# Performance work log

Measured on AMD Instinct MI355X. Metric: run time of the kernel, lower is better.

## Reference

```python
import jax, jax.numpy as jnp
import numpy as np

B, N, E, H = 8, 10000, 320000, 128


def setup_inputs() -> dict:
    key = jax.random.key(0)
    ks = jax.random.split(key, 8)
    x = jax.random.normal(ks[0], (B, N, H), dtype=jnp.float32)
    adj_val = jnp.ones((B, E), dtype=jnp.float32)
    src = jax.random.randint(ks[1], (B, E), 0, N, dtype=jnp.int32)
    dst = jax.random.randint(ks[2], (B, E), 0, N, dtype=jnp.int32)
    scale = 0.05  # 'random_normal' keras initializer default stddev
    W_t = scale * jax.random.normal(ks[3], (H, H), dtype=jnp.float32)
    b_t = jnp.zeros((H,), dtype=jnp.float32)
    W_h = scale * jax.random.normal(ks[4], (H, H), dtype=jnp.float32)
    theta = scale * jax.random.normal(ks[5], (H, H), dtype=jnp.float32)
    return {"x": x, "adj_val": adj_val, "src": src, "dst": dst,
            "W_t": W_t, "b_t": b_t, "W_h": W_h, "theta": theta}


def reference(x, adj_val, src, dst, W_t, b_t, W_h, theta):
    # adj is sparse [B, N, N]: adj[b, src[b,e], dst[b,e]] = adj_val[b,e]
    n = x.shape[1]
    # in_degrees = row-sums of adj
    deg = jax.vmap(lambda v, s: jax.ops.segment_sum(v, s, num_segments=n))(adj_val, src)
    norm = jnp.power(deg + 1e-6, -0.5)[..., None]            # [B, N, 1]
    f_hom = jnp.einsum('bnh,hk->bnk', x, theta) * norm       # [B, N, H]
    # batched SpMM: out[b,i] = sum_e adj_val[b,e] * y[b, dst[b,e]] into row src[b,e]
    def spmm(v, s, d, y):
        return jax.ops.segment_sum(v[:, None] * y[d], s, num_segments=n)
    f_hom = jax.vmap(spmm)(adj_val, src, dst, f_hom) * norm  # [B, N, H]
    f_het = jnp.einsum('bnh,hk->bnk', x, W_h)
    gate = jax.nn.sigmoid(jnp.einsum('bnh,hk->bnk', x, W_t) + b_t)
    return gate * f_hom + (1.0 - gate) * f_het
```

## Files before the change

### kernel.cpp

```cpp
#include <hip/hip_runtime.h>

#define BATCH 8
#define NNODE 10000
#define NEDGE 320000
#define HD    128
#define NROW  (BATCH * NNODE)
#define NEDG_TOT (BATCH * NEDGE)
#define LDW 136
#define KB  32
#define CEB (NEDGE / KB)
#define G   64
#define NBUCK 157
#define NBP 160
#define NBT (BATCH * NBP)
#define WCVT_B 192

typedef __attribute__((ext_vector_type(8))) short short8;
typedef __attribute__((ext_vector_type(4))) float f32x4;

__device__ __forceinline__ short f2bf(float f) {
    unsigned u = __float_as_uint(f);
    unsigned r = u + 0x7FFFu + ((u >> 16) & 1u);
    return (short)(r >> 16);
}
__device__ __forceinline__ float bflo(unsigned y) { return __uint_as_float(y << 16); }
__device__ __forceinline__ float bfhi(unsigned y) { return __uint_as_float(y & 0xffff0000u); }

__global__ __launch_bounds__(512) void k_hist(const int* __restrict__ src,
                                              int* __restrict__ cc) {
    __shared__ int scc[NBP];
    int t = threadIdx.x, blk = blockIdx.x;
    if (t < NBP) scc[t] = 0;
    __syncthreads();
    int b = blk >> 5, kb = blk & (KB - 1);
    long e0 = (long)b * NEDGE + (long)kb * CEB;
    for (int i0 = t; i0 < CEB; i0 += 2048) {
        int i1 = i0 + 512, i2 = i0 + 1024, i3 = i0 + 1536;
        int s0 = src[e0 + i0];
        int s1 = (i1 < CEB) ? src[e0 + i1] : -1;
        int s2 = (i2 < CEB) ? src[e0 + i2] : -1;
        int s3 = (i3 < CEB) ? src[e0 + i3] : -1;
        atomicAdd(&scc[s0 >> 6], 1);
        if (s1 >= 0) atomicAdd(&scc[s1 >> 6], 1);
        if (s2 >= 0) atomicAdd(&scc[s2 >> 6], 1);
        if (s3 >= 0) atomicAdd(&scc[s3 >> 6], 1);
    }
    __syncthreads();
    if (t < NBP) cc[blk * NBP + t] = scc[t];
}

__global__ __launch_bounds__(256) void k_misc(const float* __restrict__ th,
                                              const float* __restrict__ Wt,
                                              const float* __restrict__ Wh,
                                              short* __restrict__ wbf,
                                              int* __restrict__ cc,
                                              int* __restrict__ tot_c,
                                              int* __restrict__ cbaseA,
                                              int* __restrict__ cbaseB) {
    __shared__ int partA[256], partB[256];
    int t = threadIdx.x, blk = blockIdx.x;
    if (blk < WCVT_B) {
        int i = blk * 256 + t;
        int w = i >> 14, idx = i & 16383;
        int n = idx >> 7, k = idx & 127;
        const float* W = (w == 0) ? th : ((w == 1) ? Wt : Wh);
        wbf[i] = f2bf(W[k * HD + n]);
    } else {
        int tot[5], locA[5], locB[5]; int runA = 0, runB = 0;
        #pragma unroll
        for (int j = 0; j < 5; ++j) {
            int gi = t * 5 + j, b = gi / NBP, bk = gi % NBP;
            int s = 0;
            for (int k = 0; k < KB; ++k) s += cc[(b * KB + k) * NBP + bk];
            tot[j] = s;
            locA[j] = runA; runA += s;
            locB[j] = runB; runB += (s + 3 * G + 3) & ~3;
        }
        partA[t] = runA; partB[t] = runB; __syncthreads();
        for (int off = 1; off < 256; off <<= 1) {
            int a = partA[t], bb = partB[t];
            int aa = (t >= off) ? partA[t - off] : 0;
            int ab = (t >= off) ? partB[t - off] : 0;
            __syncthreads();
            partA[t] = a + aa; partB[t] = bb + ab;
            __syncthreads();
        }
        int exA = (t == 0) ? 0 : partA[t - 1];
        int exB = (t == 0) ? 0 : partB[t - 1];
        #pragma unroll
        for (int j = 0; j < 5; ++j) {
            int gi = t * 5 + j, b = gi / NBP, bk = gi % NBP;
            tot_c[gi]  = tot[j];
            cbaseA[gi] = exA + locA[j];
            cbaseB[gi] = exB + locB[j];
            int run2 = exA + locA[j];
            for (int k = 0; k < KB; ++k) {
                int idx = (b * KB + k) * NBP + bk;
                int c = cc[idx];
                cc[idx] = run2;
                run2 += c;
            }
        }
    }
}

__global__ __launch_bounds__(512) void k_scatA(const float* __restrict__ adj,
                                               const int* __restrict__ src,
                                               const int* __restrict__ dst,
                                               const int* __restrict__ cbases,
                                               int2* __restrict__ epairA) {
    __shared__ int cur[NBP];
    int t = threadIdx.x, blk = blockIdx.x;
    if (t < NBP) cur[t] = cbases[blk * NBP + t];
    __syncthreads();
    int b = blk >> 5, kb = blk & (KB - 1);
    long e0 = (long)b * NEDGE + (long)kb * CEB;
    for (int i0 = t; i0 < CEB; i0 += 2048) {
        int i1 = i0 + 512, i2 = i0 + 1024, i3 = i0 + 1536;
        int s0 = src[e0 + i0], d0 = dst[e0 + i0];
        float a0 = adj[e0 + i0];
        int s1 = -1, d1 = 0; float a1 = 0.f;
        int s2 = -1, d2 = 0; float a2 = 0.f;
        int s3 = -1, d3 = 0; float a3 = 0.f;
        if (i1 < CEB) { s1 = src[e0 + i1]; d1 = dst[e0 + i1]; a1 = adj[e0 + i1]; }
        if (i2 < CEB) { s2 = src[e0 + i2]; d2 = dst[e0 + i2]; a2 = adj[e0 + i2]; }
        if (i3 < CEB) { s3 = src[e0 + i3]; d3 = dst[e0 + i3]; a3 = adj[e0 + i3]; }
        int p0 = atomicAdd(&cur[s0 >> 6], 1);
        epairA[p0] = make_int2((s0 << 16) | d0, __float_as_int(a0));
        if (s1 >= 0) {
            int p1 = atomicAdd(&cur[s1 >> 6], 1);
            epairA[p1] = make_int2((s1 << 16) | d1, __float_as_int(a1));
        }
        if (s2 >= 0) {
            int p2 = atomicAdd(&cur[s2 >> 6], 1);
            epairA[p2] = make_int2((s2 << 16) | d2, __float_as_int(a2));
        }
        if (s3 >= 0) {
            int p3 = atomicAdd(&cur[s3 >> 6], 1);
            epairA[p3] = make_int2((s3 << 16) | d3, __float_as_int(a3));
        }
    }
}

__global__ __launch_bounds__(256) void k_refine(const int* __restrict__ cbaseA,
                                                const int* __restrict__ cbaseB,
                                                const int* __restrict__ tot_c,
                                                const int2* __restrict__ epairA,
                                                int* __restrict__ rowptr,
                                                int* __restrict__ total,
                                                float* __restrict__ norm,
                                                int* __restrict__ epakB) {
    __shared__ int   rcnt[G];
    __shared__ float sdeg[G];
    __shared__ int   rcur[G];
    int t = threadIdx.x;
    int batch = blockIdx.x & 7, bk = blockIdx.x >> 3;
    if (t < G) { rcnt[t] = 0; sdeg[t] = 0.f; }
    __syncthreads();
    int gi = batch * NBP + bk;
    int p0 = cbaseA[gi], n = tot_c[gi], pB = cbaseB[gi];
    for (int i = t; i < n; i += 256) {
        int2 e = epairA[p0 + i];
        int rl = (e.x >> 16) & (G - 1);
        atomicAdd(&rcnt[rl], 1);
        atomicAdd(&sdeg[rl], __int_as_float(e.y));
    }
    __syncthreads();
    if (t < G) {
        int v = rcnt[t];
        int pv = (v + 3) & ~3;
        int inc = pv;
        #pragma unroll
        for (int off = 1; off < G; off <<= 1) {
            int u = __shfl_up(inc, off, G);
            if (t >= off) inc += u;
        }
        int start = pB + inc - pv;
        rcur[t] = start;
        int node = bk * G + t;
        if (node < NNODE) {
            long r = (long)batch * NNODE + node;
            rowptr[r] = start;
            total[r] = v;
            norm[r] = rsqrtf(sdeg[t] + 1e-6f);
        }
    }
    __syncthreads();
    for (int i = t; i < n; i += 256) {
        int2 e = epairA[p0 + i];
        int rl = (e.x >> 16) & (G - 1);
        int p = atomicAdd(&rcur[rl], 1);
        unsigned vbf = (unsigned short)f2bf(__int_as_float(e.y));
        epakB[p] = (e.x & 0xffff) | (vbf << 16);
    }
}

__global__ __launch_bounds__(256) void k_gemm3(const float* __restrict__ x,
                                               const short* __restrict__ wbf,
                                               const float* __restrict__ norm,
                                               const float* __restrict__ bt,
                                               short* __restrict__ Y,
                                               unsigned* __restrict__ outgh) {
    __shared__ short lb[2 * HD * LDW];
    int tx = threadIdx.x;
    for (int i = tx; i < HD * 16; i += 256) {
        int n = i >> 4, kc = (i & 15) << 3;
        *(float4*)(&lb[n * LDW + kc])            = *(const float4*)(&wbf[n * HD + kc]);
        *(float4*)(&lb[HD * LDW + n * LDW + kc]) = *(const float4*)(&wbf[16384 + n * HD + kc]);
    }
    __syncthreads();

    int wv = tx >> 6, l = tx & 63;
    long row0 = (long)blockIdx.x * 64 + wv * 16;
    int mrow = l & 15, kg = l >> 4;
    const float* xp = x + (row0 + mrow) * HD + kg * 8;

    f32x4 ac0[8], ac1[8];
    #pragma unroll
    for (int f = 0; f < 8; ++f) { ac0[f] = (f32x4){0.f,0.f,0.f,0.f}; ac1[f] = (f32x4){0.f,0.f,0.f,0.f}; }

    #pragma unroll
    for (int c = 0; c < 4; ++c) {
        float4 a0 = *(const float4*)(xp + c * 32);
        float4 a1 = *(const float4*)(xp + c * 32 + 4);
        short8 a;
        a[0]=f2bf(a0.x); a[1]=f2bf(a0.y); a[2]=f2bf(a0.z); a[3]=f2bf(a0.w);
        a[4]=f2bf(a1.x); a[5]=f2bf(a1.y); a[6]=f2bf(a1.z); a[7]=f2bf(a1.w);
        #pragma unroll
        for (int f = 0; f < 8; ++f) {
            short8 b0 = *(short8*)(&lb[(16 * f + mrow) * LDW + c * 32 + kg * 8]);
            short8 b1 = *(short8*)(&lb[HD * LDW + (16 * f + mrow) * LDW + c * 32 + kg * 8]);
            ac0[f] = __builtin_amdgcn_mfma_f32_16x16x32_bf16(a, b0, ac0[f], 0, 0, 0);
            ac1[f] = __builtin_amdgcn_mfma_f32_16x16x32_bf16(a, b1, ac1[f], 0, 0, 0);
        }
    }
    float nr[4];
    #pragma unroll
    for (int r = 0; r < 4; ++r) nr[r] = norm[row0 + kg * 4 + r];
    #pragma unroll
    for (int f = 0; f < 8; ++f)
        #pragma unroll
        for (int r = 0; r < 4; ++r)
            Y[(row0 + kg * 4 + r) * HD + 16 * f + mrow] = f2bf(ac0[f][r] * nr[r]);

    __syncthreads();
    for (int i = tx; i < HD * 16; i += 256) {
        int n = i >> 4, kc = (i & 15) << 3;
        *(float4*)(&lb[n * LDW + kc]) = *(const float4*)(&wbf[2 * 16384 + n * HD + kc]);
    }
    __syncthreads();

    f32x4 ac2[8];
    #pragma unroll
    for (int f = 0; f < 8; ++f) ac2[f] = (f32x4){0.f,0.f,0.f,0.f};
    #pragma unroll
    for (int c = 0; c < 4; ++c) {
        float4 a0 = *(const float4*)(xp + c * 32);
        float4 a1 = *(const float4*)(xp + c * 32 + 4);
        short8 a;
        a[0]=f2bf(a0.x); a[1]=f2bf(a0.y); a[2]=f2bf(a0.z); a[3]=f2bf(a0.w);
        a[4]=f2bf(a1.x); a[5]=f2bf(a1.y); a[6]=f2bf(a1.z); a[7]=f2bf(a1.w);
        #pragma unroll
        for (int f = 0; f < 8; ++f) {
            short8 b = *(short8*)(&lb[(16 * f + mrow) * LDW + c * 32 + kg * 8]);
            ac2[f] = __builtin_amdgcn_mfma_f32_16x16x32_bf16(a, b, ac2[f], 0, 0, 0);
        }
    }
    #pragma unroll
    for (int f = 0; f < 8; ++f) {
        float bb = bt[16 * f + mrow];
        #pragma unroll
        for (int r = 0; r < 4; ++r) {
            long idx = (row0 + kg * 4 + r) * HD + 16 * f + mrow;
            float g = 1.f / (1.f + __expf(-(ac1[f][r] + bb)));
            unsigned glo = (unsigned short)f2bf(g);
            unsigned hhi = (unsigned short)f2bf(ac2[f][r]);
            outgh[idx] = glo | (hhi << 16);
        }
    }
}

__global__ __launch_bounds__(256) void k_gather(const int* __restrict__ rowptr,
                                                const int* __restrict__ total,
                                                const int* __restrict__ epak,
                                                const short* __restrict__ Y,
                                                const float* __restrict__ norm,
                                                float* __restrict__ out) {
    int batch = blockIdx.x & 7;
    int ib    = blockIdx.x >> 3;
    int wave = threadIdx.x >> 6, lane = threadIdx.x & 63;
    long r = (long)batch * NNODE + ib * 4 + wave;
    const short* Yb = Y + (long)batch * NNODE * HD + 2 * lane;
    int p0 = __builtin_amdgcn_readfirstlane(rowptr[r]);
    int n  = __builtin_amdgcn_readfirstlane(total[r]);
    const int* ep = epak + p0;
    float ax = 0.f, ay = 0.f;
    int i = 0;
    for (; i + 16 <= n; i += 16) {
        int4 mA = *(const int4*)(ep + i);
        int4 mB = *(const int4*)(ep + i + 4);
        int4 mC = *(const int4*)(ep + i + 8);
        int4 mD = *(const int4*)(ep + i + 12);
        unsigned y0 = *(const unsigned*)(Yb + (long)(mA.x & 0xffff) * HD);
        unsigned y1 = *(const unsigned*)(Yb + (long)(mA.y & 0xffff) * HD);
        unsigned y2 = *(const unsigned*)(Yb + (long)(mA.z & 0xffff) * HD);
        unsigned y3 = *(const unsigned*)(Yb + (long)(mA.w & 0xffff) * HD);
        unsigned y4 = *(const unsigned*)(Yb + (long)(mB.x & 0xffff) * HD);
        unsigned y5 = *(const unsigned*)(Yb + (long)(mB.y & 0xffff) * HD);
        unsigned y6 = *(const unsigned*)(Yb + (long)(mB.z & 0xffff) * HD);
        unsigned y7 = *(const unsigned*)(Yb + (long)(mB.w & 0xffff) * HD);
        unsigned y8 = *(const unsigned*)(Yb + (long)(mC.x & 0xffff) * HD);
        unsigned y9 = *(const unsigned*)(Yb + (long)(mC.y & 0xffff) * HD);
        unsigned yA = *(const unsigned*)(Yb + (long)(mC.z & 0xffff) * HD);
        unsigned yB = *(const unsigned*)(Yb + (long)(mC.w & 0xffff) * HD);
        unsigned yC = *(const unsigned*)(Yb + (long)(mD.x & 0xffff) * HD);
        unsigned yD = *(const unsigned*)(Yb + (long)(mD.y & 0xffff) * HD);
        unsigned yE = *(const unsigned*)(Yb + (long)(mD.z & 0xffff) * HD);
        unsigned yF = *(const unsigned*)(Yb + (long)(mD.w & 0xffff) * HD);
        float v0 = bfhi((unsigned)mA.x), v1 = bfhi((unsigned)mA.y);
        float v2 = bfhi((unsigned)mA.z), v3 = bfhi((unsigned)mA.w);
        float v4 = bfhi((unsigned)mB.x), v5 = bfhi((unsigned)mB.y);
        float v6 = bfhi((unsigned)mB.z), v7 = bfhi((unsigned)mB.w);
        float v8 = bfhi((unsigned)mC.x), v9 = bfhi((unsigned)mC.y);
        float vA = bfhi((unsigned)mC.z), vB = bfhi((unsigned)mC.w);
        float vC = bfhi((unsigned)mD.x), vD = bfhi((unsigned)mD.y);
        float vE = bfhi((unsigned)mD.z), vF = bfhi((unsigned)mD.w);
        ax += v0 * bflo(y0); ay += v0 * bfhi(y0);
        ax += v1 * bflo(y1); ay += v1 * bfhi(y1);
        ax += v2 * bflo(y2); ay += v2 * bfhi(y2);
        ax += v3 * bflo(y3); ay += v3 * bfhi(y3);
        ax += v4 * bflo(y4); ay += v4 * bfhi(y4);
        ax += v5 * bflo(y5); ay += v5 * bfhi(y5);
        ax += v6 * bflo(y6); ay += v6 * bfhi(y6);
        ax += v7 * bflo(y7); ay += v7 * bfhi(y7);
        ax += v8 * bflo(y8); ay += v8 * bfhi(y8);
        ax += v9 * bflo(y9); ay += v9 * bfhi(y9);
        ax += vA * bflo(yA); ay += vA * bfhi(yA);
        ax += vB * bflo(yB); ay += vB * bfhi(yB);
        ax += vC * bflo(yC); ay += vC * bfhi(yC);
        ax += vD * bflo(yD); ay += vD * bfhi(yD);
        ax += vE * bflo(yE); ay += vE * bfhi(yE);
        ax += vF * bflo(yF); ay += vF * bfhi(yF);
    }
    for (; i + 4 <= n; i += 4) {
        int4 mA = *(const int4*)(ep + i);
        unsigned y0 = *(const unsigned*)(Yb + (long)(mA.x & 0xffff) * HD);
        unsigned y1 = *(const unsigned*)(Yb + (long)(mA.y & 0xffff) * HD);
        unsigned y2 = *(const unsigned*)(Yb + (long)(mA.z & 0xffff) * HD);
        unsigned y3 = *(const unsigned*)(Yb + (long)(mA.w & 0xffff) * HD);
        float v0 = bfhi((unsigned)mA.x), v1 = bfhi((unsigned)mA.y);
        float v2 = bfhi((unsigned)mA.z), v3 = bfhi((unsigned)mA.w);
        ax += v0 * bflo(y0); ay += v0 * bfhi(y0);
        ax += v1 * bflo(y1); ay += v1 * bfhi(y1);
        ax += v2 * bflo(y2); ay += v2 * bfhi(y2);
        ax += v3 * bflo(y3); ay += v3 * bfhi(y3);
    }
    for (; i < n; ++i) {
        unsigned e = (unsigned)ep[i];
        unsigned y = *(const unsigned*)(Yb + (long)(e & 0xffff) * HD);
        float v = bfhi(e);
        ax += v * bflo(y); ay += v * bfhi(y);
    }
    float nrm = norm[r];
    uint2 gh = ((const uint2*)(out + r * HD))[lane];
    float g0 = bflo(gh.x), h0 = bfhi(gh.x);
    float g1 = bflo(gh.y), h1 = bfhi(gh.y);
    float z0 = ax * nrm, z1 = ay * nrm;
    ((float2*)(out + r * HD))[lane] =
        make_float2(g0 * z0 + (1.f - g0) * h0, g1 * z1 + (1.f - g1) * h1);
}

extern "C" void kernel_launch(void* const* d_in, const int* in_sizes, int n_in,
                              void* d_out, int out_size, void* d_ws, size_t ws_size,
                              hipStream_t stream) {
    const float* x     = (const float*)d_in[0];
    const float* adj   = (const float*)d_in[1];
    const int*   src   = (const int*)d_in[2];
    const int*   dst   = (const int*)d_in[3];
    const float* Wt    = (const float*)d_in[4];
    const float* bt    = (const float*)d_in[5];
    const float* Wh    = (const float*)d_in[6];
    const float* theta = (const float*)d_in[7];
    float* out = (float*)d_out;

    char* p = (char*)d_ws;
    float* norm   = (float*)p;  p += (size_t)NROW * 4;
    int*   total  = (int*)p;    p += (size_t)NROW * 4;
    int*   rowptr = (int*)p;    p += (size_t)NROW * 4;
    int*   tot_c  = (int*)p;    p += (size_t)NBT * 4;
    int*   cbaseA = (int*)p;    p += (size_t)NBT * 4;
    int*   cbaseB = (int*)p;    p += (size_t)NBT * 4;
    int*   cc     = (int*)p;    p += (size_t)BATCH * KB * NBP * 4;
    short* wbf    = (short*)p;  p += 3 * 16384 * 2;
    int2*  epairA = (int2*)p;
    short* Y      = (short*)p;  p += (size_t)NROW * HD * 2;
    int*   epakB  = (int*)p;    p += (size_t)(NEDG_TOT + NBT * 256) * 4;

    k_hist  <<<BATCH * KB, 512, 0, stream>>>(src, cc);
    k_misc  <<<WCVT_B + 1, 256, 0, stream>>>(theta, Wt, Wh, wbf, cc, tot_c, cbaseA, cbaseB);
    k_scatA <<<BATCH * KB, 512, 0, stream>>>(adj, src, dst, cc, epairA);
    k_refine<<<BATCH * NBUCK, 256, 0, stream>>>(cbaseA, cbaseB, tot_c, epairA,
                                                rowptr, total, norm, epakB);
    k_gemm3 <<<NROW / 64, 256, 0, stream>>>(x, wbf, norm, bt, Y, (unsigned*)out);
    k_gather<<<NROW / 4, 256, 0, stream>>>(rowptr, total, epakB, Y, norm, out);
}
```

Baseline: 152.7 us.

## Run GEMM phases sequentially with one LDS weight buffer and cached bf16 A fragments

The fused three-weight GEMM kernel now loads one 128x128 bf16 weight matrix into LDS at a time, halving shared memory, and runs the theta, W_t and W_h products one after another with a single accumulator set. The x rows are converted to bf16 once and held in registers instead of being reloaded and reconverted for the last GEMM, and gate values are packed into 16 registers between phases. This lowers LDS and accumulator register use to allow more resident blocks, at the cost of extra barriers and serialized weight loads.

```diff
diff --git a/kernel.cpp b/kernel.cpp
--- a/kernel.cpp
+++ b/kernel.cpp
@@ -201,24 +201,14 @@
                                                const float* __restrict__ bt,
                                                short* __restrict__ Y,
                                                unsigned* __restrict__ outgh) {
-    __shared__ short lb[2 * HD * LDW];
+    __shared__ short lb[HD * LDW];
     int tx = threadIdx.x;
-    for (int i = tx; i < HD * 16; i += 256) {
-        int n = i >> 4, kc = (i & 15) << 3;
-        *(float4*)(&lb[n * LDW + kc])            = *(const float4*)(&wbf[n * HD + kc]);
-        *(float4*)(&lb[HD * LDW + n * LDW + kc]) = *(const float4*)(&wbf[16384 + n * HD + kc]);
-    }
-    __syncthreads();
-
     int wv = tx >> 6, l = tx & 63;
     long row0 = (long)blockIdx.x * 64 + wv * 16;
     int mrow = l & 15, kg = l >> 4;
     const float* xp = x + (row0 + mrow) * HD + kg * 8;
 
-    f32x4 ac0[8], ac1[8];
-    #pragma unroll
-    for (int f = 0; f < 8; ++f) { ac0[f] = (f32x4){0.f,0.f,0.f,0.f}; ac1[f] = (f32x4){0.f,0.f,0.f,0.f}; }
-
+    short8 af[4];
     #pragma unroll
     for (int c = 0; c < 4; ++c) {
         float4 a0 = *(const float4*)(xp + c * 32);
@@ -226,14 +216,24 @@
         short8 a;
         a[0]=f2bf(a0.x); a[1]=f2bf(a0.y); a[2]=f2bf(a0.z); a[3]=f2bf(a0.w);
         a[4]=f2bf(a1.x); a[5]=f2bf(a1.y); a[6]=f2bf(a1.z); a[7]=f2bf(a1.w);
+        af[c] = a;
+    }
+
+    for (int i = tx; i < HD * 16; i += 256) {
+        int n = i >> 4, kc = (i & 15) << 3;
+        *(float4*)(&lb[n * LDW + kc]) = *(const float4*)(&wbf[n * HD + kc]);
+    }
+    __syncthreads();
+    f32x4 ac[8];
+    #pragma unroll
+    for (int f = 0; f < 8; ++f) ac[f] = (f32x4){0.f,0.f,0.f,0.f};
+    #pragma unroll
+    for (int c = 0; c < 4; ++c)
         #pragma unroll
         for (int f = 0; f < 8; ++f) {
-            short8 b0 = *(short8*)(&lb[(16 * f + mrow) * LDW + c * 32 + kg * 8]);
-            short8 b1 = *(short8*)(&lb[HD * LDW + (16 * f + mrow) * LDW + c * 32 + kg * 8]);
-            ac0[f] = __builtin_amdgcn_mfma_f32_16x16x32_bf16(a, b0, ac0[f], 0, 0, 0);
-            ac1[f] = __builtin_amdgcn_mfma_f32_16x16x32_bf16(a, b1, ac1[f], 0, 0, 0);
-        }
-    }
+            short8 b = *(short8*)(&lb[(16 * f + mrow) * LDW + c * 32 + kg * 8]);
+            ac[f] = __builtin_amdgcn_mfma_f32_16x16x32_bf16(af[c], b, ac[f], 0, 0, 0);
+        }
     float nr[4];
     #pragma unroll
     for (int r = 0; r < 4; ++r) nr[r] = norm[row0 + kg * 4 + r];
@@ -241,7 +241,36 @@
     for (int f = 0; f < 8; ++f)
         #pragma unroll
         for (int r = 0; r < 4; ++r)
-            Y[(row0 + kg * 4 + r) * HD + 16 * f + mrow] = f2bf(ac0[f][r] * nr[r]);
+            Y[(row0 + kg * 4 + r) * HD + 16 * f + mrow] = f2bf(ac[f][r] * nr[r]);
+
+    __syncthreads();
+    for (int i = tx; i < HD * 16; i += 256) {
+        int n = i >> 4, kc = (i & 15) << 3;
+        *(float4*)(&lb[n * LDW + kc]) = *(const float4*)(&wbf[16384 + n * HD + kc]);
+    }
+    __syncthreads();
+    #pragma unroll
+    for (int f = 0; f < 8; ++f) ac[f] = (f32x4){0.f,0.f,0.f,0.f};
+    #pragma unroll
+    for (int c = 0; c < 4; ++c)
+        #pragma unroll
+        for (int f = 0; f < 8; ++f) {
+            short8 b = *(short8*)(&lb[(16 * f + mrow) * LDW + c * 32 + kg * 8]);
+            ac[f] = __builtin_amdgcn_mfma_f32_16x16x32_bf16(af[c], b, ac[f], 0, 0, 0);
+        }
+    unsigned g16[16];
+    #pragma unroll
+    for (int f = 0; f < 8; ++f) {
+        float bb = bt[16 * f + mrow];
+        #pragma unroll
+        for (int r = 0; r < 4; ++r) {
+            int q = f * 4 + r;
+            float g = 1.f / (1.f + __expf(-(ac[f][r] + bb)));
+            unsigned gb = (unsigned short)f2bf(g);
+            if (q & 1) g16[q >> 1] |= gb << 16;
+            else       g16[q >> 1]  = gb;
+        }
+    }
 
     __syncthreads();
     for (int i = tx; i < HD * 16; i += 256) {
@@ -249,35 +278,25 @@
         *(float4*)(&lb[n * LDW + kc]) = *(const float4*)(&wbf[2 * 16384 + n * HD + kc]);
     }
     __syncthreads();
-
-    f32x4 ac2[8];
-    #pragma unroll
-    for (int f = 0; f < 8; ++f) ac2[f] = (f32x4){0.f,0.f,0.f,0.f};
-    #pragma unroll
-    for (int c = 0; c < 4; ++c) {
-        float4 a0 = *(const float4*)(xp + c * 32);
-        float4 a1 = *(const float4*)(xp + c * 32 + 4);
-        short8 a;
-        a[0]=f2bf(a0.x); a[1]=f2bf(a0.y); a[2]=f2bf(a0.z); a[3]=f2bf(a0.w);
-        a[4]=f2bf(a1.x); a[5]=f2bf(a1.y); a[6]=f2bf(a1.z); a[7]=f2bf(a1.w);
+    #pragma unroll
+    for (int f = 0; f < 8; ++f) ac[f] = (f32x4){0.f,0.f,0.f,0.f};
+    #pragma unroll
+    for (int c = 0; c < 4; ++c)
         #pragma unroll
         for (int f = 0; f < 8; ++f) {
             short8 b = *(short8*)(&lb[(16 * f + mrow) * LDW + c * 32 + kg * 8]);
-            ac2[f] = __builtin_amdgcn_mfma_f32_16x16x32_bf16(a, b, ac2[f], 0, 0, 0);
-        }
-    }
-    #pragma unroll
-    for (int f = 0; f < 8; ++f) {
-        float bb = bt[16 * f + mrow];
+            ac[f] = __builtin_amdgcn_mfma_f32_16x16x32_bf16(af[c], b, ac[f], 0, 0, 0);
+        }
+    #pragma unroll
+    for (int f = 0; f < 8; ++f)
         #pragma unroll
         for (int r = 0; r < 4; ++r) {
+            int q = f * 4 + r;
             long idx = (row0 + kg * 4 + r) * HD + 16 * f + mrow;
-            float g = 1.f / (1.f + __expf(-(ac1[f][r] + bb)));
-            unsigned glo = (unsigned short)f2bf(g);
-            unsigned hhi = (unsigned short)f2bf(ac2[f][r]);
-            outgh[idx] = glo | (hhi << 16);
-        }
-    }
+            unsigned gb = (q & 1) ? (g16[q >> 1] >> 16) : (g16[q >> 1] & 0xffffu);
+            unsigned hhi = (unsigned short)f2bf(ac[f][r]);
+            outgh[idx] = gb | (hhi << 16);
+        }
 }
 
 __global__ __launch_bounds__(256) void k_gather(const int* __restrict__ rowptr,
```

Result: faster. 146.1 us (-4.3%).
